# Performance work log

Hardware: AMD Instinct MI355X
Metric: run time of the kernel (lower is better)

The kernel has to match this reference:

```python
import jax, jax.numpy as jnp
import numpy as np

B, S, D, VOCAB = 64, 2048, 256, 32000


def setup_inputs() -> dict:
    key = jax.random.key(0)
    k1, k2, k3 = jax.random.split(key, 3)
    chunk = jax.random.randint(k1, (B, S), 0, VOCAB, dtype=jnp.int32)
    encoding = jax.random.normal(k2, (B, S, D), dtype=jnp.float32)
    # idf weights are positive; uniform (0,1] avoids zero-sum pathologies
    idf = jax.random.uniform(k3, (VOCAB,), dtype=jnp.float32, minval=1e-3, maxval=1.0)
    return {"chunk": chunk, "encoding": encoding, "idf": idf}


def reference(chunk, encoding, idf):
    """Batched, fused version of DocumentDualEmbedder.get_doc_embedding.

    chunk:    [B, S] int token ids
    encoding: [B, S, D] transformer outputs
    idf:      [vocab] idf weight table
    returns:  [B, 4*D] (idf-weighted mean | max | min | std)
    """
    seq_len = encoding.shape[1]
    w = idf[chunk]                                  # [B, S] gather
    w = w / jnp.sum(w, axis=1, keepdims=True)       # per-doc normalize
    mean_emb = jnp.einsum('bs,bsd->bd', w, encoding)
    max_emb = jnp.max(encoding, axis=1)
    min_emb = jnp.min(encoding, axis=1)
    # torch.std default: unbiased (divide by S-1)
    mu = jnp.mean(encoding, axis=1, keepdims=True)  # [B, 1, D]
    var = jnp.sum(jnp.square(encoding - mu), axis=1) / (seq_len - 1)
    std_emb = jnp.sqrt(var)
    return jnp.concatenate([mean_emb, max_emb, min_emb, std_emb], axis=-1)
```

## Files before the change

### kernel.cpp

```cpp
#include <hip/hip_runtime.h>

#define BB 64
#define SS 2048
#define DD 256
#define NQ 4
#define DQ (DD / NQ)
#define NT 1024
#define NW (NT / 64)

#define FLT_BIG 3.4028234e38f

__global__ __launch_bounds__(NT) void fused_kernel(
    const int* __restrict__ chunk, const float* __restrict__ enc,
    const float* __restrict__ idf, float* __restrict__ out) {
  const int dq = blockIdx.x;
  const int b = blockIdx.y;
  const int tid = threadIdx.x;
  const int lane = tid & 63;
  const int wid = tid >> 6;
  const int d4 = tid & 15;
  const int srow = tid >> 4;

  __shared__ float sw[SS];
  __shared__ float warr[NW];
  __shared__ float red[NW][16][20];

  float w0 = idf[chunk[b * SS + tid]];
  float w1 = idf[chunk[b * SS + NT + tid]];
  sw[tid] = w0;
  sw[NT + tid] = w1;
  float wp = w0 + w1;
#pragma unroll
  for (int off = 32; off > 0; off >>= 1) wp += __shfl_down(wp, off, 64);
  if (lane == 0) warr[wid] = wp;
  __syncthreads();

  float swe[4] = {0.f, 0.f, 0.f, 0.f};
  float se[4] = {0.f, 0.f, 0.f, 0.f};
  float se2[4] = {0.f, 0.f, 0.f, 0.f};
  float mx[4], mn[4];
#pragma unroll
  for (int k = 0; k < 4; k++) {
    mx[k] = -FLT_BIG;
    mn[k] = FLT_BIG;
  }

  const float* base = enc + ((size_t)b * SS) * DD + dq * DQ + d4 * 4;
#pragma unroll 8
  for (int k = 0; k < SS / 64; k++) {
    int s = srow + 64 * k;
    float w = sw[s];
    float4 e = *(const float4*)(base + (size_t)s * DD);
    float ev[4] = {e.x, e.y, e.z, e.w};
#pragma unroll
    for (int j = 0; j < 4; j++) {
      swe[j] = fmaf(w, ev[j], swe[j]);
      se[j] += ev[j];
      se2[j] = fmaf(ev[j], ev[j], se2[j]);
      mx[j] = fmaxf(mx[j], ev[j]);
      mn[j] = fminf(mn[j], ev[j]);
    }
  }

#pragma unroll
  for (int j = 0; j < 4; j++) {
    swe[j] += __shfl_xor(swe[j], 32, 64);
    swe[j] += __shfl_xor(swe[j], 16, 64);
    se[j] += __shfl_xor(se[j], 32, 64);
    se[j] += __shfl_xor(se[j], 16, 64);
    se2[j] += __shfl_xor(se2[j], 32, 64);
    se2[j] += __shfl_xor(se2[j], 16, 64);
    mx[j] = fmaxf(mx[j], __shfl_xor(mx[j], 32, 64));
    mx[j] = fmaxf(mx[j], __shfl_xor(mx[j], 16, 64));
    mn[j] = fminf(mn[j], __shfl_xor(mn[j], 32, 64));
    mn[j] = fminf(mn[j], __shfl_xor(mn[j], 16, 64));
  }
  if (lane < 16) {
    float* r = red[wid][lane];
#pragma unroll
    for (int j = 0; j < 4; j++) {
      r[j] = swe[j];
      r[4 + j] = se[j];
      r[8 + j] = se2[j];
      r[12 + j] = mx[j];
      r[16 + j] = mn[j];
    }
  }
  __syncthreads();

  if (tid < DQ) {
    int f4 = tid >> 2, comp = tid & 3;
    float cswe = 0.f, cse = 0.f, cse2 = 0.f, wtot = 0.f;
    float cmx = -FLT_BIG, cmn = FLT_BIG;
#pragma unroll
    for (int wv = 0; wv < NW; wv++) {
      const float* r = red[wv][f4];
      cswe += r[comp];
      cse += r[4 + comp];
      cse2 += r[8 + comp];
      cmx = fmaxf(cmx, r[12 + comp]);
      cmn = fminf(cmn, r[16 + comp]);
      wtot += warr[wv];
    }
    float mu = cse / (float)SS;
    float stdv =
        sqrtf(fmaxf((cse2 - (float)SS * mu * mu) / (float)(SS - 1), 0.f));
    int d = dq * DQ + tid;
    size_t ob = (size_t)b * 4 * DD;
    out[ob + d] = cswe / wtot;
    out[ob + DD + d] = cmx;
    out[ob + 2 * DD + d] = cmn;
    out[ob + 3 * DD + d] = stdv;
  }
}

extern "C" void kernel_launch(void* const* d_in, const int* in_sizes, int n_in,
                              void* d_out, int out_size, void* d_ws,
                              size_t ws_size, hipStream_t stream) {
  const int* chunk = (const int*)d_in[0];
  const float* enc = (const float*)d_in[1];
  const float* idf = (const float*)d_in[2];
  float* out = (float*)d_out;

  fused_kernel<<<dim3(NQ, BB), NT, 0, stream>>>(chunk, enc, idf, out);
}
```

Before: 199.2 us.

## Double-buffer encoding loads with nontemporal prefetch overlapping idf gather

Issues the first batch of eight float4 encoding loads before the idf gather and its weight reduction, then alternates two register buffers so each group's loads are in flight while the previous group is processed. Loads use nontemporal hints so the streamed encoding data is marked as not worth caching. This is meant to hide global memory latency and overlap the dependent chunk-to-idf gather with the main stream. The cost is extra register pressure from 64 live floats, at a 1024-thread block size.

```diff
diff --git a/kernel.cpp b/kernel.cpp
--- a/kernel.cpp
+++ b/kernel.cpp
@@ -9,6 +9,8 @@
 #define NW (NT / 64)
 
 #define FLT_BIG 3.4028234e38f
+
+typedef float f32x4 __attribute__((ext_vector_type(4)));
 
 __global__ __launch_bounds__(NT) void fused_kernel(
     const int* __restrict__ chunk, const float* __restrict__ enc,
@@ -25,8 +27,23 @@
   __shared__ float warr[NW];
   __shared__ float red[NW][16][20];
 
-  float w0 = idf[chunk[b * SS + tid]];
-  float w1 = idf[chunk[b * SS + NT + tid]];
+  const int c0 = chunk[b * SS + tid];
+  const int c1 = chunk[b * SS + NT + tid];
+
+  const float* base = enc + ((size_t)b * SS) * DD + dq * DQ + d4 * 4;
+
+  f32x4 bufA[8], bufB[8];
+
+#define LOADG(buf, g)                                                        \
+  _Pragma("unroll") for (int k = 0; k < 8; ++k) {                            \
+    buf[k] = __builtin_nontemporal_load(                                     \
+        (const f32x4*)(base + (size_t)(srow + 64 * (8 * (g) + k)) * DD));    \
+  }
+
+  LOADG(bufA, 0)
+
+  float w0 = idf[c0];
+  float w1 = idf[c1];
   sw[tid] = w0;
   sw[NT + tid] = w1;
   float wp = w0 + w1;
@@ -45,22 +62,30 @@
     mn[k] = FLT_BIG;
   }
 
-  const float* base = enc + ((size_t)b * SS) * DD + dq * DQ + d4 * 4;
-#pragma unroll 8
-  for (int k = 0; k < SS / 64; k++) {
-    int s = srow + 64 * k;
-    float w = sw[s];
-    float4 e = *(const float4*)(base + (size_t)s * DD);
-    float ev[4] = {e.x, e.y, e.z, e.w};
-#pragma unroll
-    for (int j = 0; j < 4; j++) {
-      swe[j] = fmaf(w, ev[j], swe[j]);
-      se[j] += ev[j];
-      se2[j] = fmaf(ev[j], ev[j], se2[j]);
-      mx[j] = fmaxf(mx[j], ev[j]);
-      mn[j] = fminf(mn[j], ev[j]);
-    }
+#define PROCG(buf, g)                                                        \
+  _Pragma("unroll") for (int k = 0; k < 8; ++k) {                            \
+    const int s = srow + 64 * (8 * (g) + k);                                 \
+    const float w = sw[s];  \
+    _Pragma("unroll") for (int j = 0; j < 4; ++j) {                          \
+      const float e = buf[k][j];                                             \
+      swe[j] = fmaf(w, e, swe[j]);                                           \
+      se[j] += e;                                                            \
+      se2[j] = fmaf(e, e, se2[j]);                                           \
+      mx[j] = fmaxf(mx[j], e);                                               \
+      mn[j] = fminf(mn[j], e);                                               \
+    }                                                                        \
   }
+
+  LOADG(bufB, 1)
+  PROCG(bufA, 0)
+  LOADG(bufA, 2)
+  PROCG(bufB, 1)
+  LOADG(bufB, 3)
+  PROCG(bufA, 2)
+  PROCG(bufB, 3)
+
+#undef LOADG
+#undef PROCG
 
 #pragma unroll
   for (int j = 0; j < 4; j++) {
```

New measurement: 185.6 us, median of 2. 1.07x faster.
